# Kernel tuning notes

Hardware: AMD Instinct MI355X
Metric: run time of the kernel (lower is better)

The kernel has to match this reference:

```python
import jax, jax.numpy as jnp
import numpy as np

LN_EPS = 1e-5
NORM_EPS = 1e-12  # F.normalize eps


def _l2norm(x):
    # torch F.normalize(p=2, dim=-1): x / max(||x||, eps)
    n = jnp.sqrt(jnp.sum(x * x, axis=-1, keepdims=True))
    return x / jnp.maximum(n, NORM_EPS)


def setup_inputs() -> dict:
    key = jax.random.key(0)
    D, R, H = 256, 32, 64  # d_model, rank, d_model//4
    B, C, P = 32, 64, 96
    ks = jax.random.split(key, 16)
    s = 0.05
    return {
        "x": jax.random.normal(ks[0], (B * C, P, D), jnp.float32),
        "ln_gamma": jnp.ones((D,), jnp.float32),
        "ln_beta": jnp.zeros((D,), jnp.float32),
        "Wd": jax.random.normal(ks[1], (D, R), jnp.float32) * s,
        "bd": jax.random.normal(ks[2], (R,), jnp.float32) * s,
        "Wq": jax.random.normal(ks[3], (R, R), jnp.float32) * s,
        "Wk": jax.random.normal(ks[4], (R, R), jnp.float32) * s,
        "Wv": jax.random.normal(ks[5], (R, R), jnp.float32) * s,
        "Wg": jax.random.normal(ks[6], (R, R), jnp.float32) * s,
        "bg": jax.random.normal(ks[7], (R,), jnp.float32) * s,
        "Wu": jax.random.normal(ks[8], (R, D), jnp.float32) * s,
        "bu": jax.random.normal(ks[9], (D,), jnp.float32) * s,
        "W1": jax.random.normal(ks[10], (D, H), jnp.float32) * s,
        "b1": jax.random.normal(ks[11], (H,), jnp.float32) * s,
        "W2": jax.random.normal(ks[12], (H, D), jnp.float32) * s,
        "b2": jnp.full((D,), -5.0, jnp.float32),  # gate_init bias
        "B": B,
        "C": C,
    }


def reference(x, ln_gamma, ln_beta, Wd, bd, Wq, Wk, Wv, Wg, bg, Wu, bu, W1, b1, W2, b2, B, C):
    BC, P, D = x.shape
    # [B*C, P, D] -> [B*P, C, D] channel-mixing layout
    h = x.reshape(B, C, P, D).transpose(0, 2, 1, 3).reshape(B * P, C, D)

    # LayerNorm over D (biased variance, as in torch LayerNorm)
    mu = jnp.mean(h, axis=-1, keepdims=True)
    var = jnp.var(h, axis=-1, keepdims=True)
    h_norm = (h - mu) * jax.lax.rsqrt(var + LN_EPS) * ln_gamma + ln_beta

    # bottleneck projection to rank R
    h_low = h_norm @ Wd + bd  # [BP, C, R]

    # Hydra linear attention: cosine-normalized Q/K, sum-pooled K*V global feature
    Q = _l2norm(h_low @ Wq)
    K = _l2norm(h_low @ Wk)
    V = h_low @ Wv
    global_feat = jnp.sum(K * V, axis=1, keepdims=True)  # [BP, 1, R]
    h_attn = Q * global_feat

    # content gate and up-projection
    gate_c = jax.nn.sigmoid(h_low @ Wg + bg)
    mixed = (h_attn * gate_c) @ Wu + bu  # [BP, C, D]

    # AdaptiveGate: unbiased variance over channel dim (torch .var default ddof=1)
    chan_var = jnp.var(h, axis=1, ddof=1)  # [BP, D]
    gate_logits = jax.nn.gelu(chan_var @ W1 + b1, approximate=False) @ W2 + b2
    gate = jax.nn.sigmoid(gate_logits)[:, None, :]  # [BP, 1, D]

    out = h + gate * mixed
    # back to [B*C, P, D]
    return out.reshape(B, P, C, D).transpose(0, 2, 1, 3).reshape(BC, P, D)
```

## Files before the change

### kernel.cpp

```cpp
#include <hip/hip_runtime.h>

#define DD 256
#define RR 32
#define CC 64
#define PB 96
#define NT 1024

typedef __attribute__((ext_vector_type(8))) short short8;
typedef __attribute__((ext_vector_type(4))) float f32x4;

__device__ __forceinline__ unsigned short f2b(float f) {
    union { float f; unsigned u; } v; v.f = f;
    unsigned r = v.u + 0x7fffu + ((v.u >> 16) & 1u);
    return (unsigned short)(r >> 16);
}
__device__ __forceinline__ float b2f(unsigned short s) {
    union { unsigned u; float f; } v; v.u = ((unsigned)s) << 16;
    return v.f;
}

__device__ __forceinline__ int hidx(int c, int d) {
    return c * 256 + ((((d >> 3) ^ (c & 7)) << 3) | (d & 7));
}
__device__ __forceinline__ int nidx(int row, int k) {
    return row * 32 + ((((k >> 3) ^ ((row >> 1) & 3)) << 3) | (k & 7));
}

__global__ __launch_bounds__(1024, 1)
void prep_kernel(const float* __restrict__ ln_g, const float* __restrict__ ln_b,
                 const float* __restrict__ Wd, const float* __restrict__ bd,
                 const float* __restrict__ Wq, const float* __restrict__ Wk,
                 const float* __restrict__ Wv, const float* __restrict__ Wg,
                 const float* __restrict__ Wu,
                 short* __restrict__ wsWd, short* __restrict__ wsQKVG,
                 short* __restrict__ wsWu, float* __restrict__ wsLN)
{
    __shared__ float redp[2048];
    const int t = threadIdx.x;
    {
        const int r = t >> 5, dblk = t & 31;
        short8 vv;
        float sa = 0.f, sb = 0.f;
        #pragma unroll
        for (int j = 0; j < 8; ++j) {
            const int d = dblk * 8 + j;
            const float wd = Wd[d * RR + r];
            const float g  = ln_g[d];
            vv[j] = (short)f2b(g * wd);
            sa += g * wd;
            sb += ln_b[d] * wd;
        }
        *(short8*)&wsWd[r * 256 + ((dblk ^ (r & 7)) << 3)] = vv;
        redp[r * 32 + dblk]        = sa;
        redp[1024 + r * 32 + dblk] = sb;
    }
    if (t < 512) {
        const int m = t >> 7, rr2 = (t >> 2) & 31, kg = t & 3;
        const float* Wm = (m == 0) ? Wq : (m == 1) ? Wk : (m == 2) ? Wv : Wg;
        short8 vv;
        #pragma unroll
        for (int j = 0; j < 8; ++j)
            vv[j] = (short)f2b(Wm[(kg * 8 + j) * RR + rr2]);
        *(short8*)&wsQKVG[m * 1024 + rr2 * 32 + ((kg ^ ((rr2 >> 1) & 3)) << 3)] = vv;
    }
    {
        const int d = t & 255, kg = t >> 8;
        short8 vv;
        #pragma unroll
        for (int j = 0; j < 8; ++j)
            vv[j] = (short)f2b(Wu[(kg * 8 + j) * DD + d]);
        *(short8*)&wsWu[d * 32 + ((kg ^ ((d >> 1) & 3)) << 3)] = vv;
    }
    __syncthreads();
    if (t < 32) {
        float s = 0.f;
        #pragma unroll
        for (int g = 0; g < 32; ++g) s += redp[t * 32 + g];
        wsLN[t] = s;
    } else if (t < 64) {
        const int r = t - 32;
        float s = 0.f;
        #pragma unroll
        for (int g = 0; g < 32; ++g) s += redp[1024 + r * 32 + g];
        wsLN[t] = s + bd[r];
    }
}

__global__ __launch_bounds__(NT, 8)
void hydra_kernel(const float* __restrict__ x,
                  const short* __restrict__ wsWd, const short* __restrict__ wsQKVG,
                  const short* __restrict__ wsWu, const float* __restrict__ wsLN,
                  const float* __restrict__ bg,
                  const float* __restrict__ bu,
                  const float* __restrict__ W1, const float* __restrict__ b1,
                  const float* __restrict__ W2, const float* __restrict__ b2,
                  float* __restrict__ out)
{
    __shared__ short hbf[CC * DD];
    __shared__ short wreg[RR * DD / 2];
    __shared__ short qg[CC * RR];
    __shared__ short lowbuf[CC * RR];
    __shared__ float redA[1024];
    __shared__ float redB[2048];
    __shared__ float mu_s[CC], rstd_s[CC];
    __shared__ float cv_s[DD], gate_s[DD];
    __shared__ float hid_s[64];
    __shared__ float ln_a[RR], ln_bv[RR];

    const int t    = threadIdx.x;
    const int lane = t & 63;
    const int w    = t >> 6;
    const int bp   = blockIdx.x;
    const int b    = bp / PB;
    const int p    = bp - b * PB;
    const size_t rowbase = (size_t)(b * CC) * PB * DD + (size_t)p * DD;

    #pragma unroll
    for (int i = 0; i < 4; ++i) {
        const int c = w * 4 + i;
        const float4 v = *(const float4*)(x + rowbase + (size_t)c * (PB * DD) + 4 * lane);
        float s1 = v.x + v.y + v.z + v.w;
        float s2 = v.x * v.x + v.y * v.y + v.z * v.z + v.w * v.w;
        #pragma unroll
        for (int off = 32; off; off >>= 1) {
            s1 += __shfl_xor(s1, off, 64);
            s2 += __shfl_xor(s2, off, 64);
        }
        if (lane == 0) {
            const float mu = s1 * (1.f / 256.f);
            mu_s[c]   = mu;
            rstd_s[c] = rsqrtf(s2 * (1.f / 256.f) - mu * mu + 1e-5f);
        }
        ushort4 pk;
        pk.x = f2b(v.x); pk.y = f2b(v.y); pk.z = f2b(v.z); pk.w = f2b(v.w);
        *(ushort4*)&hbf[hidx(c, 4 * lane)] = pk;
    }
    *(short8*)&wreg[t * 8] = *(const short8*)&wsWd[t * 8];
    if (t < 32)              ln_a[t]       = wsLN[t];
    else if (t < 64)         ln_bv[t - 32] = wsLN[t];
    __syncthreads();

    f32x4 s3acc = {0.f, 0.f, 0.f, 0.f};
    if (w < 8) {
        const int ct = w >> 1, rt = w & 1;
        const int arow = ct * 16 + (lane & 15);
        const int brow = rt * 16 + (lane & 15);
        const int ksub = lane >> 4;
        #pragma unroll
        for (int step = 0; step < 8; ++step) {
            const int kb = step * 4 + ksub;
            const short8 a  = *(const short8*)&hbf[arow * 256 + ((kb ^ (arow & 7)) << 3)];
            const short8 bf = *(const short8*)&wreg[brow * 256 + ((kb ^ (brow & 7)) << 3)];
            s3acc = __builtin_amdgcn_mfma_f32_16x16x32_bf16(a, bf, s3acc, 0, 0, 0);
        }
    } else {
        const int idx = t - 512;
        const int dp  = idx & 127;
        const int rg  = idx >> 7;
        const int d0  = dp * 2;
        float s1a = 0.f, s1b = 0.f, s2a = 0.f, s2b = 0.f;
        #pragma unroll 4
        for (int i = 0; i < 16; ++i) {
            const int c = rg * 16 + i;
            const ushort2 u = *(const ushort2*)&hbf[hidx(c, d0)];
            const float va = b2f(u.x), vb = b2f(u.y);
            s1a += va; s2a += va * va;
            s1b += vb; s2b += vb * vb;
        }
        *(float2*)&redB[rg * 256 + d0]        = make_float2(s1a, s1b);
        *(float2*)&redB[1024 + rg * 256 + d0] = make_float2(s2a, s2b);
    }
    __syncthreads();

    if (w < 8) {
        const int ct = w >> 1, rt = w & 1;
        const int col = rt * 16 + (lane & 15);
        const float la = ln_a[col], lb = ln_bv[col];
        #pragma unroll
        for (int i = 0; i < 4; ++i) {
            const int c = ct * 16 + (lane >> 4) * 4 + i;
            const float rs = rstd_s[c];
            const float hl = rs * s3acc[i] - rs * mu_s[c] * la + lb;
            lowbuf[nidx(c, col)] = (short)f2b(hl);
        }
    } else {
        const int idx = t - 512;
        *(short8*)&wreg[idx * 8] = *(const short8*)&wsQKVG[idx * 8];
    }
    if (t < 256) {
        const float S1 = redB[t] + redB[256 + t] + redB[512 + t] + redB[768 + t];
        const float S2 = redB[1024 + t] + redB[1280 + t] + redB[1536 + t] + redB[1792 + t];
        cv_s[t] = (S2 - S1 * S1 * (1.f / 64.f)) * (1.f / 63.f);
    }
    __syncthreads();

    if (w < 8) {
        const int ct = w >> 1, pair = w & 1;
        const int mA = pair ? 1 : 0;
        const int mB = pair ? 2 : 3;
        const int arow = ct * 16 + (lane & 15);
        const int ksub = lane >> 4;
        const short8 a = *(const short8*)&lowbuf[arow * 32 + ((ksub ^ ((arow >> 1) & 3)) << 3)];
        f32x4 aA0 = {0,0,0,0}, aA1 = {0,0,0,0}, aB0 = {0,0,0,0}, aB1 = {0,0,0,0};
        {
            const int br0 = (lane & 15), br1 = 16 + (lane & 15);
            const short8 bA0 = *(const short8*)&wreg[mA * 1024 + br0 * 32 + ((ksub ^ ((br0 >> 1) & 3)) << 3)];
            const short8 bA1 = *(const short8*)&wreg[mA * 1024 + br1 * 32 + ((ksub ^ ((br1 >> 1) & 3)) << 3)];
            const short8 bB0 = *(const short8*)&wreg[mB * 1024 + br0 * 32 + ((ksub ^ ((br0 >> 1) & 3)) << 3)];
            const short8 bB1 = *(const short8*)&wreg[mB * 1024 + br1 * 32 + ((ksub ^ ((br1 >> 1) & 3)) << 3)];
            aA0 = __builtin_amdgcn_mfma_f32_16x16x32_bf16(a, bA0, aA0, 0, 0, 0);
            aA1 = __builtin_amdgcn_mfma_f32_16x16x32_bf16(a, bA1, aA1, 0, 0, 0);
            aB0 = __builtin_amdgcn_mfma_f32_16x16x32_bf16(a, bB0, aB0, 0, 0, 0);
            aB1 = __builtin_amdgcn_mfma_f32_16x16x32_bf16(a, bB1, aB1, 0, 0, 0);
        }
        float qs[4];
        #pragma unroll
        for (int i = 0; i < 4; ++i) {
            float ss = aA0[i] * aA0[i] + aA1[i] * aA1[i];
            ss += __shfl_xor(ss, 1, 64);
            ss += __shfl_xor(ss, 2, 64);
            ss += __shfl_xor(ss, 4, 64);
            ss += __shfl_xor(ss, 8, 64);
            qs[i] = 1.f / fmaxf(sqrtf(ss), 1e-12f);
        }
        const int col0 = (lane & 15), col1 = 16 + (lane & 15);
        if (pair == 0) {
            const float bgv0 = bg[col0], bgv1 = bg[col1];
            #pragma unroll
            for (int i = 0; i < 4; ++i) {
                const int c = ct * 16 + (lane >> 4) * 4 + i;
                const float g0 = 1.f / (1.f + __expf(-(aB0[i] + bgv0)));
                const float g1 = 1.f / (1.f + __expf(-(aB1[i] + bgv1)));
                qg[c * 32 + col0] = (short)f2b(aA0[i] * qs[i] * g0);
                qg[c * 32 + col1] = (short)f2b(aA1[i] * qs[i] * g1);
            }
        } else {
            #pragma unroll
            for (int i = 0; i < 4; ++i) {
                const int c = ct * 16 + (lane >> 4) * 4 + i;
                redB[c * 32 + col0] = aA0[i] * qs[i] * aB0[i];
                redB[c * 32 + col1] = aA1[i] * qs[i] * aB1[i];
            }
        }
    } else {
        const int idx = t - 512;
        const int j = idx & 63, dg = idx >> 6;
        float s = 0.f;
        #pragma unroll 8
        for (int i = 0; i < 32; ++i) {
            const int d = dg * 32 + i;
            s += cv_s[d] * W1[d * 64 + j];
        }
        redA[dg * 64 + j] = s;
    }
    __syncthreads();

    if (t < 64) {
        float s = b1[t];
        #pragma unroll
        for (int g = 0; g < 8; ++g) s += redA[g * 64 + t];
        hid_s[t] = 0.5f * s * (1.f + erff(s * 0.70710678118654752f));
    }
    if (t >= 256 && t < 512) {
        const int idx = t - 256;
        const int r = idx & 31, g = idx >> 5;
        float s = 0.f;
        #pragma unroll
        for (int i = 0; i < 8; ++i)
            s += redB[(g * 8 + i) * 32 + r];
        redA[512 + g * 32 + r] = s;
    }
    *(short8*)&wreg[t * 8] = *(const short8*)&wsWu[t * 8];
    __syncthreads();

    {
        const int d = t & 255, jg = t >> 8;
        float s = 0.f;
        #pragma unroll
        for (int i = 0; i < 16; ++i) {
            const int j = jg * 16 + i;
            s += hid_s[j] * W2[j * DD + d];
        }
        redB[jg * 256 + d] = s;
    }
    if (t < 256) {
        const int r = t & 31, c0 = t >> 5, c1 = (t >> 5) + 32;
        float gf = 0.f;
        #pragma unroll
        for (int g = 0; g < 8; ++g) gf += redA[512 + g * 32 + r];
        lowbuf[nidx(c0, r)] = (short)f2b(b2f((unsigned short)qg[c0 * 32 + r]) * gf);
        lowbuf[nidx(c1, r)] = (short)f2b(b2f((unsigned short)qg[c1 * 32 + r]) * gf);
    }
    __syncthreads();

    {
        const int ct = w & 3, dg = w >> 2;
        const int arow = ct * 16 + (lane & 15);
        const int ksub = lane >> 4;
        const short8 a = *(const short8*)&lowbuf[arow * 32 + ((ksub ^ ((arow >> 1) & 3)) << 3)];
        #pragma unroll
        for (int j = 0; j < 4; ++j) {
            const int dt = dg * 4 + j;
            const int col = dt * 16 + (lane & 15);
            const short8 bf = *(const short8*)&wreg[col * 32 + ((ksub ^ ((col >> 1) & 3)) << 3)];
            f32x4 acc = {0.f, 0.f, 0.f, 0.f};
            acc = __builtin_amdgcn_mfma_f32_16x16x32_bf16(a, bf, acc, 0, 0, 0);
            #pragma unroll
            for (int i = 0; i < 4; ++i) {
                const int c = ct * 16 + (lane >> 4) * 4 + i;
                hbf[hidx(c, col)] = (short)f2b(acc[i]);
            }
        }
    }
    if (t < 256) {
        const float s = redB[t] + redB[256 + t] + redB[512 + t] + redB[768 + t] + b2[t];
        gate_s[t] = 1.f / (1.f + __expf(-s));
    }
    __syncthreads();

    #pragma unroll
    for (int i = 0; i < 4; ++i) {
        const int c = w * 4 + i;
        const size_t off = rowbase + (size_t)c * (PB * DD) + 4 * lane;
        const float4 xv = *(const float4*)(x + off);
        const ushort4 m = *(const ushort4*)&hbf[hidx(c, 4 * lane)];
        const float4 g4 = *(const float4*)&gate_s[4 * lane];
        const float4 bu4 = *(const float4*)(bu + 4 * lane);
        float4 o;
        o.x = xv.x + g4.x * (b2f(m.x) + bu4.x);
        o.y = xv.y + g4.y * (b2f(m.y) + bu4.y);
        o.z = xv.z + g4.z * (b2f(m.z) + bu4.z);
        o.w = xv.w + g4.w * (b2f(m.w) + bu4.w);
        *(float4*)(out + off) = o;
    }
}

extern "C" void kernel_launch(void* const* d_in, const int* in_sizes, int n_in,
                              void* d_out, int out_size, void* d_ws, size_t ws_size,
                              hipStream_t stream) {
    (void)in_sizes; (void)n_in; (void)out_size; (void)ws_size;
    const float* x    = (const float*)d_in[0];
    const float* ln_g = (const float*)d_in[1];
    const float* ln_b = (const float*)d_in[2];
    const float* Wd   = (const float*)d_in[3];
    const float* bd   = (const float*)d_in[4];
    const float* Wq   = (const float*)d_in[5];
    const float* Wk   = (const float*)d_in[6];
    const float* Wv   = (const float*)d_in[7];
    const float* Wg   = (const float*)d_in[8];
    const float* bg   = (const float*)d_in[9];
    const float* Wu   = (const float*)d_in[10];
    const float* bu   = (const float*)d_in[11];
    const float* W1   = (const float*)d_in[12];
    const float* b1   = (const float*)d_in[13];
    const float* W2   = (const float*)d_in[14];
    const float* b2   = (const float*)d_in[15];
    float* out = (float*)d_out;

    short* wsWd   = (short*)d_ws;
    short* wsQKVG = wsWd + 8192;
    short* wsWu   = wsQKVG + 4096;
    float* wsLN   = (float*)(wsWd + 20480);

    prep_kernel<<<dim3(1), dim3(1024), 0, stream>>>(
        ln_g, ln_b, Wd, bd, Wq, Wk, Wv, Wg, Wu, wsWd, wsQKVG, wsWu, wsLN);
    hydra_kernel<<<dim3(32 * PB), dim3(NT), 0, stream>>>(
        x, wsWd, wsQKVG, wsWu, wsLN, bg, bu, W1, b1, W2, b2, out);
}
```

Baseline: 139.7 us.

## Pre-transpose gate MLP weights and vectorize matvecs, shorten LN shuffle reduction

The prep kernel now writes transposed copies of W1 and W2 so the gate MLP matvecs in the main kernel can use contiguous float4 loads instead of strided scalar loads. The per-row LayerNorm reduction uses only three shuffle steps and finishes through a new shared buffer in the second phase. Float-to-bf16 conversion switches to the HIP intrinsic, and the swizzle index helpers are simplified. Shared memory use grows (wreg doubled, new redC), which may lower blocks per CU.

```diff
diff --git a/kernel.cpp b/kernel.cpp
--- a/kernel.cpp
+++ b/kernel.cpp
@@ -1,4 +1,5 @@
 #include <hip/hip_runtime.h>
+#include <hip/hip_bf16.h>
 
 #define DD 256
 #define RR 32
@@ -9,21 +10,19 @@
 typedef __attribute__((ext_vector_type(8))) short short8;
 typedef __attribute__((ext_vector_type(4))) float f32x4;
 
-__device__ __forceinline__ unsigned short f2b(float f) {
-    union { float f; unsigned u; } v; v.f = f;
-    unsigned r = v.u + 0x7fffu + ((v.u >> 16) & 1u);
-    return (unsigned short)(r >> 16);
+__device__ __forceinline__ short f2bf(float f) {
+    return __builtin_bit_cast(short, __float2bfloat16(f));
 }
 __device__ __forceinline__ float b2f(unsigned short s) {
     union { unsigned u; float f; } v; v.u = ((unsigned)s) << 16;
     return v.f;
 }
 
-__device__ __forceinline__ int hidx(int c, int d) {
-    return c * 256 + ((((d >> 3) ^ (c & 7)) << 3) | (d & 7));
-}
-__device__ __forceinline__ int nidx(int row, int k) {
-    return row * 32 + ((((k >> 3) ^ ((row >> 1) & 3)) << 3) | (k & 7));
+__device__ __forceinline__ int hswz(int c, int d) {
+    return c * 256 + (d ^ ((c & 7) << 3));
+}
+__device__ __forceinline__ int nswz(int r, int k) {
+    return r * 32 + (k ^ (((r >> 1) & 3) << 3));
 }
 
 __global__ __launch_bounds__(1024, 1)
@@ -32,8 +31,10 @@
                  const float* __restrict__ Wq, const float* __restrict__ Wk,
                  const float* __restrict__ Wv, const float* __restrict__ Wg,
                  const float* __restrict__ Wu,
+                 const float* __restrict__ W1, const float* __restrict__ W2,
                  short* __restrict__ wsWd, short* __restrict__ wsQKVG,
-                 short* __restrict__ wsWu, float* __restrict__ wsLN)
+                 short* __restrict__ wsWu, float* __restrict__ wsLN,
+                 float* __restrict__ wsW1T, float* __restrict__ wsW2T)
 {
     __shared__ float redp[2048];
     const int t = threadIdx.x;
@@ -46,7 +47,7 @@
             const int d = dblk * 8 + j;
             const float wd = Wd[d * RR + r];
             const float g  = ln_g[d];
-            vv[j] = (short)f2b(g * wd);
+            vv[j] = f2bf(g * wd);
             sa += g * wd;
             sb += ln_b[d] * wd;
         }
@@ -60,7 +61,7 @@
         short8 vv;
         #pragma unroll
         for (int j = 0; j < 8; ++j)
-            vv[j] = (short)f2b(Wm[(kg * 8 + j) * RR + rr2]);
+            vv[j] = f2bf(Wm[(kg * 8 + j) * RR + rr2]);
         *(short8*)&wsQKVG[m * 1024 + rr2 * 32 + ((kg ^ ((rr2 >> 1) & 3)) << 3)] = vv;
     }
     {
@@ -68,8 +69,20 @@
         short8 vv;
         #pragma unroll
         for (int j = 0; j < 8; ++j)
-            vv[j] = (short)f2b(Wu[(kg * 8 + j) * DD + d]);
+            vv[j] = f2bf(Wu[(kg * 8 + j) * DD + d]);
         *(short8*)&wsWu[d * 32 + ((kg ^ ((d >> 1) & 3)) << 3)] = vv;
+    }
+    #pragma unroll
+    for (int rep = 0; rep < 16; ++rep) {
+        const int id = rep * 1024 + t;
+        const int j = id >> 8, d = id & 255;
+        wsW1T[j * 256 + d] = W1[d * 64 + j];
+    }
+    #pragma unroll
+    for (int rep = 0; rep < 16; ++rep) {
+        const int id = rep * 1024 + t;
+        const int d = id >> 6, j = id & 63;
+        wsW2T[d * 64 + j] = W2[j * 256 + d];
     }
     __syncthreads();
     if (t < 32) {
@@ -90,18 +103,19 @@
 void hydra_kernel(const float* __restrict__ x,
                   const short* __restrict__ wsWd, const short* __restrict__ wsQKVG,
                   const short* __restrict__ wsWu, const float* __restrict__ wsLN,
+                  const float* __restrict__ wsW1T, const float* __restrict__ wsW2T,
                   const float* __restrict__ bg,
                   const float* __restrict__ bu,
-                  const float* __restrict__ W1, const float* __restrict__ b1,
-                  const float* __restrict__ W2, const float* __restrict__ b2,
+                  const float* __restrict__ b1, const float* __restrict__ b2,
                   float* __restrict__ out)
 {
     __shared__ short hbf[CC * DD];
-    __shared__ short wreg[RR * DD / 2];
+    __shared__ short wreg[RR * DD];
     __shared__ short qg[CC * RR];
     __shared__ short lowbuf[CC * RR];
     __shared__ float redA[1024];
     __shared__ float redB[2048];
+    __shared__ float redC[1024];
     __shared__ float mu_s[CC], rstd_s[CC];
     __shared__ float cv_s[DD], gate_s[DD];
     __shared__ float hid_s[64];
@@ -121,19 +135,15 @@
         const float4 v = *(const float4*)(x + rowbase + (size_t)c * (PB * DD) + 4 * lane);
         float s1 = v.x + v.y + v.z + v.w;
         float s2 = v.x * v.x + v.y * v.y + v.z * v.z + v.w * v.w;
-        #pragma unroll
-        for (int off = 32; off; off >>= 1) {
-            s1 += __shfl_xor(s1, off, 64);
-            s2 += __shfl_xor(s2, off, 64);
-        }
-        if (lane == 0) {
-            const float mu = s1 * (1.f / 256.f);
-            mu_s[c]   = mu;
-            rstd_s[c] = rsqrtf(s2 * (1.f / 256.f) - mu * mu + 1e-5f);
-        }
+        s1 += __shfl_xor(s1, 1, 64); s2 += __shfl_xor(s2, 1, 64);
+        s1 += __shfl_xor(s1, 2, 64); s2 += __shfl_xor(s2, 2, 64);
+        s1 += __shfl_xor(s1, 4, 64); s2 += __shfl_xor(s2, 4, 64);
+        if ((lane & 7) == 0)
+            *(float2*)&redC[(c * 8 + (lane >> 3)) * 2] = make_float2(s1, s2);
         ushort4 pk;
-        pk.x = f2b(v.x); pk.y = f2b(v.y); pk.z = f2b(v.z); pk.w = f2b(v.w);
-        *(ushort4*)&hbf[hidx(c, 4 * lane)] = pk;
+        pk.x = (unsigned short)f2bf(v.x); pk.y = (unsigned short)f2bf(v.y);
+        pk.z = (unsigned short)f2bf(v.z); pk.w = (unsigned short)f2bf(v.w);
+        *(ushort4*)&hbf[hswz(c, 4 * lane)] = pk;
     }
     *(short8*)&wreg[t * 8] = *(const short8*)&wsWd[t * 8];
     if (t < 32)              ln_a[t]       = wsLN[t];
@@ -148,9 +158,8 @@
         const int ksub = lane >> 4;
         #pragma unroll
         for (int step = 0; step < 8; ++step) {
-            const int kb = step * 4 + ksub;
-            const short8 a  = *(const short8*)&hbf[arow * 256 + ((kb ^ (arow & 7)) << 3)];
-            const short8 bf = *(const short8*)&wreg[brow * 256 + ((kb ^ (brow & 7)) << 3)];
+            const short8 a  = *(const short8*)&hbf[hswz(arow, step * 32 + ksub * 8)];
+            const short8 bf = *(const short8*)&wreg[hswz(brow, step * 32 + ksub * 8)];
             s3acc = __builtin_amdgcn_mfma_f32_16x16x32_bf16(a, bf, s3acc, 0, 0, 0);
         }
     } else {
@@ -159,16 +168,28 @@
         const int rg  = idx >> 7;
         const int d0  = dp * 2;
         float s1a = 0.f, s1b = 0.f, s2a = 0.f, s2b = 0.f;
-        #pragma unroll 4
+        #pragma unroll
         for (int i = 0; i < 16; ++i) {
             const int c = rg * 16 + i;
-            const ushort2 u = *(const ushort2*)&hbf[hidx(c, d0)];
+            const ushort2 u = *(const ushort2*)&hbf[hswz(c, d0)];
             const float va = b2f(u.x), vb = b2f(u.y);
             s1a += va; s2a += va * va;
             s1b += vb; s2b += vb * vb;
         }
         *(float2*)&redB[rg * 256 + d0]        = make_float2(s1a, s1b);
         *(float2*)&redB[1024 + rg * 256 + d0] = make_float2(s2a, s2b);
+        if (idx < 64) {
+            const int c = idx;
+            float s1 = 0.f, s2 = 0.f;
+            #pragma unroll
+            for (int g = 0; g < 8; ++g) {
+                const float2 pr = *(const float2*)&redC[(c * 8 + g) * 2];
+                s1 += pr.x; s2 += pr.y;
+            }
+            const float mu = s1 * (1.f / 256.f);
+            mu_s[c]   = mu;
+            rstd_s[c] = rsqrtf(s2 * (1.f / 256.f) - mu * mu + 1e-5f);
+        }
     }
     __syncthreads();
 
@@ -181,7 +202,7 @@
             const int c = ct * 16 + (lane >> 4) * 4 + i;
             const float rs = rstd_s[c];
             const float hl = rs * s3acc[i] - rs * mu_s[c] * la + lb;
-            lowbuf[nidx(c, col)] = (short)f2b(hl);
+            lowbuf[nswz(c, col)] = f2bf(hl);
         }
     } else {
         const int idx = t - 512;
@@ -200,14 +221,14 @@
         const int mB = pair ? 2 : 3;
         const int arow = ct * 16 + (lane & 15);
         const int ksub = lane >> 4;
-        const short8 a = *(const short8*)&lowbuf[arow * 32 + ((ksub ^ ((arow >> 1) & 3)) << 3)];
+        const short8 a = *(const short8*)&lowbuf[nswz(arow, ksub * 8)];
         f32x4 aA0 = {0,0,0,0}, aA1 = {0,0,0,0}, aB0 = {0,0,0,0}, aB1 = {0,0,0,0};
         {
             const int br0 = (lane & 15), br1 = 16 + (lane & 15);
-            const short8 bA0 = *(const short8*)&wreg[mA * 1024 + br0 * 32 + ((ksub ^ ((br0 >> 1) & 3)) << 3)];
-            const short8 bA1 = *(const short8*)&wreg[mA * 1024 + br1 * 32 + ((ksub ^ ((br1 >> 1) & 3)) << 3)];
-            const short8 bB0 = *(const short8*)&wreg[mB * 1024 + br0 * 32 + ((ksub ^ ((br0 >> 1) & 3)) << 3)];
-            const short8 bB1 = *(const short8*)&wreg[mB * 1024 + br1 * 32 + ((ksub ^ ((br1 >> 1) & 3)) << 3)];
+            const short8 bA0 = *(const short8*)&wreg[mA * 1024 + nswz(br0, ksub * 8)];
+            const short8 bA1 = *(const short8*)&wreg[mA * 1024 + nswz(br1, ksub * 8)];
+            const short8 bB0 = *(const short8*)&wreg[mB * 1024 + nswz(br0, ksub * 8)];
+            const short8 bB1 = *(const short8*)&wreg[mB * 1024 + nswz(br1, ksub * 8)];
             aA0 = __builtin_amdgcn_mfma_f32_16x16x32_bf16(a, bA0, aA0, 0, 0, 0);
             aA1 = __builtin_amdgcn_mfma_f32_16x16x32_bf16(a, bA1, aA1, 0, 0, 0);
             aB0 = __builtin_amdgcn_mfma_f32_16x16x32_bf16(a, bB0, aB0, 0, 0, 0);
@@ -231,8 +252,8 @@
                 const int c = ct * 16 + (lane >> 4) * 4 + i;
                 const float g0 = 1.f / (1.f + __expf(-(aB0[i] + bgv0)));
                 const float g1 = 1.f / (1.f + __expf(-(aB1[i] + bgv1)));
-                qg[c * 32 + col0] = (short)f2b(aA0[i] * qs[i] * g0);
-                qg[c * 32 + col1] = (short)f2b(aA1[i] * qs[i] * g1);
+                qg[c * 32 + col0] = f2bf(aA0[i] * qs[i] * g0);
+                qg[c * 32 + col1] = f2bf(aA1[i] * qs[i] * g1);
             }
         } else {
             #pragma unroll
@@ -245,11 +266,13 @@
     } else {
         const int idx = t - 512;
         const int j = idx & 63, dg = idx >> 6;
-        float s = 0.f;
-        #pragma unroll 8
-        for (int i = 0; i < 32; ++i) {
-            const int d = dg * 32 + i;
-            s += cv_s[d] * W1[d * 64 + j];
+        const float* w1row = wsW1T + j * 256 + dg * 32;
+        float s = 0.f;
+        #pragma unroll
+        for (int ii = 0; ii < 8; ++ii) {
+            const float4 wv = *(const float4*)(w1row + ii * 4);
+            const float4 cvv = *(const float4*)&cv_s[dg * 32 + ii * 4];
+            s += cvv.x * wv.x + cvv.y * wv.y + cvv.z * wv.z + cvv.w * wv.w;
         }
         redA[dg * 64 + j] = s;
     }
@@ -275,11 +298,13 @@
 
     {
         const int d = t & 255, jg = t >> 8;
-        float s = 0.f;
-        #pragma unroll
-        for (int i = 0; i < 16; ++i) {
-            const int j = jg * 16 + i;
-            s += hid_s[j] * W2[j * DD + d];
+        const float* w2row = wsW2T + d * 64 + jg * 16;
+        float s = 0.f;
+        #pragma unroll
+        for (int ii = 0; ii < 4; ++ii) {
+            const float4 wv = *(const float4*)(w2row + ii * 4);
+            const float4 hv = *(const float4*)&hid_s[jg * 16 + ii * 4];
+            s += hv.x * wv.x + hv.y * wv.y + hv.z * wv.z + hv.w * wv.w;
         }
         redB[jg * 256 + d] = s;
     }
@@ -288,8 +313,8 @@
         float gf = 0.f;
         #pragma unroll
         for (int g = 0; g < 8; ++g) gf += redA[512 + g * 32 + r];
-        lowbuf[nidx(c0, r)] = (short)f2b(b2f((unsigned short)qg[c0 * 32 + r]) * gf);
-        lowbuf[nidx(c1, r)] = (short)f2b(b2f((unsigned short)qg[c1 * 32 + r]) * gf);
+        lowbuf[nswz(c0, r)] = f2bf(b2f((unsigned short)qg[c0 * 32 + r]) * gf);
+        lowbuf[nswz(c1, r)] = f2bf(b2f((unsigned short)qg[c1 * 32 + r]) * gf);
     }
     __syncthreads();
 
@@ -297,18 +322,17 @@
         const int ct = w & 3, dg = w >> 2;
         const int arow = ct * 16 + (lane & 15);
         const int ksub = lane >> 4;
-        const short8 a = *(const short8*)&lowbuf[arow * 32 + ((ksub ^ ((arow >> 1) & 3)) << 3)];
+        const short8 a = *(const short8*)&lowbuf[nswz(arow, ksub * 8)];
         #pragma unroll
         for (int j = 0; j < 4; ++j) {
-            const int dt = dg * 4 + j;
-            const int col = dt * 16 + (lane & 15);
-            const short8 bf = *(const short8*)&wreg[col * 32 + ((ksub ^ ((col >> 1) & 3)) << 3)];
+            const int col = (dg * 4 + j) * 16 + (lane & 15);
+            const short8 bf = *(const short8*)&wreg[nswz(col, ksub * 8)];
             f32x4 acc = {0.f, 0.f, 0.f, 0.f};
             acc = __builtin_amdgcn_mfma_f32_16x16x32_bf16(a, bf, acc, 0, 0, 0);
             #pragma unroll
             for (int i = 0; i < 4; ++i) {
                 const int c = ct * 16 + (lane >> 4) * 4 + i;
-                hbf[hidx(c, col)] = (short)f2b(acc[i]);
+                hbf[hswz(c, col)] = f2bf(acc[i]);
             }
         }
     }
@@ -323,7 +347,7 @@
         const int c = w * 4 + i;
         const size_t off = rowbase + (size_t)c * (PB * DD) + 4 * lane;
         const float4 xv = *(const float4*)(x + off);
-        const ushort4 m = *(const ushort4*)&hbf[hidx(c, 4 * lane)];
+        const ushort4 m = *(const ushort4*)&hbf[hswz(c, 4 * lane)];
         const float4 g4 = *(const float4*)&gate_s[4 * lane];
         const float4 bu4 = *(const float4*)(bu + 4 * lane);
         float4 o;
@@ -361,9 +385,12 @@
     short* wsQKVG = wsWd + 8192;
     short* wsWu   = wsQKVG + 4096;
     float* wsLN   = (float*)(wsWd + 20480);
+    float* wsW1T  = wsLN + 64;
+    float* wsW2T  = wsW1T + 16384;
 
     prep_kernel<<<dim3(1), dim3(1024), 0, stream>>>(
-        ln_g, ln_b, Wd, bd, Wq, Wk, Wv, Wg, Wu, wsWd, wsQKVG, wsWu, wsLN);
+        ln_g, ln_b, Wd, bd, Wq, Wk, Wv, Wg, Wu, W1, W2,
+        wsWd, wsQKVG, wsWu, wsLN, wsW1T, wsW2T);
     hydra_kernel<<<dim3(32 * PB), dim3(NT), 0, stream>>>(
-        x, wsWd, wsQKVG, wsWu, wsLN, bg, bu, W1, b1, W2, b2, out);
-}
+        x, wsWd, wsQKVG, wsWu, wsLN, wsW1T, wsW2T, bg, bu, b1, b2, out);
+}
```

Result: slower. 169.7 us (+21.4%).
